# Optimization experiments

Hardware: AMD Instinct MI355X
Metric: run time of the kernel (lower is better)

## Reference

```python
import jax, jax.numpy as jnp
import numpy as np

H, FH, D = 8, 4, 64          # num_heads, focal_heads, att_size
HID = H * D                   # hidden_size = 512
B, S = 8, 512                 # batch, num_nodes
T_HOP, T_EDGE = 32, 16
SCALE = D ** -0.5


def setup_inputs() -> dict:
    key = jax.random.key(0)
    ks = jax.random.split(key, 24)
    f = lambda i, shape: jax.random.normal(ks[i], shape, jnp.float32)
    w = 1.0 / np.sqrt(HID)
    inp = {
        'q': f(0, (B, S, HID)), 'k': f(1, (B, S, HID)), 'v': f(2, (B, S, HID)),
        'query_hop_emb': f(3, (T_HOP, HID)) * 0.02,
        'query_edge_emb': f(4, (T_EDGE, HID)) * 0.02,
        'key_hop_emb': f(5, (T_HOP, HID)) * 0.02,
        'key_edge_emb': f(6, (T_EDGE, HID)) * 0.02,
        'value_hop_emb': f(7, (T_HOP, HID)) * 0.02,
        'value_edge_emb': f(8, (T_EDGE, HID)) * 0.02,
        'distance': jax.random.randint(ks[9], (B, S, S), 0, T_HOP),
        'edge_attr': jax.random.randint(ks[10], (B, S, S), 0, T_EDGE),
        # guarantee at least one unmasked key per query row to keep softmax finite
        'mask': jax.random.bernoulli(ks[11], 0.9, (B, S)).at[:, 0].set(True),
        'focal_mask': jax.random.bernoulli(ks[12], 0.5, (B, S, S)).at[:, :, 0].set(True),
        'Wq': f(13, (HID, H * D)) * w, 'bq': f(14, (H * D,)) * 0.01,
        'Wk': f(15, (HID, H * D)) * w, 'bk': f(16, (H * D,)) * 0.01,
        'Wv': f(17, (HID, H * D)) * w, 'bv': f(18, (H * D,)) * 0.01,
        'Wo': f(19, (H * D, HID)) * w, 'bo': f(20, (HID,)) * 0.01,
    }
    return inp


def _emb_scores(x, emb):
    # x: [B,H,S,D], emb: [T, H*D] -> per-head scores [B,H,S,T]
    e = emb.reshape(-1, H, D).transpose(1, 0, 2)  # [H,T,D]
    return jnp.einsum('bhsd,htd->bhst', x, e)


def _gather_last(scores, idx):
    # scores: [B,H,S,T], idx: [B,S,S] -> [B,H,S,S]
    idx_b = jnp.broadcast_to(idx[:, None], (B, H, S, S))
    return jnp.take_along_axis(scores, idx_b, axis=3)


def _scatter_add_last(attn, idx, T):
    # attn: [B,H,S,S], idx: [B,S,S] -> [B,H,S,T] accumulating attn weights
    idx_b = jnp.broadcast_to(idx[:, None], (B, H, S, S)).reshape(B * H * S, S)
    rows = jnp.arange(B * H * S)[:, None]
    flat = (rows * T + idx_b).reshape(-1)
    out = jnp.zeros((B * H * S * T,), attn.dtype).at[flat].add(attn.reshape(-1))
    return out.reshape(B, H, S, T)


def reference(q, k, v, query_hop_emb, query_edge_emb, key_hop_emb, key_edge_emb,
              value_hop_emb, value_edge_emb, distance, edge_attr, mask, focal_mask,
              Wq, bq, Wk, bk, Wv, bv, Wo, bo):
    qh = (q @ Wq + bq).reshape(B, S, H, D).transpose(0, 2, 1, 3)  # [B,H,S,D]
    kh = (k @ Wk + bk).reshape(B, S, H, D).transpose(0, 2, 1, 3)
    vh = (v @ Wv + bv).reshape(B, S, H, D).transpose(0, 2, 1, 3)

    spatial_bias = (_gather_last(_emb_scores(qh, query_hop_emb), distance)
                    + _gather_last(_emb_scores(kh, key_hop_emb), distance))
    edge_bias = (_gather_last(_emb_scores(qh, query_edge_emb), edge_attr)
                 + _gather_last(_emb_scores(kh, key_edge_emb), edge_attr))

    attn = (jnp.einsum('bhsd,bhtd->bhst', qh, kh) + spatial_bias + edge_bias) * SCALE

    GS = H - FH
    a1 = jnp.where(mask[:, None, None, :], attn[:, :GS], -jnp.inf)
    a2 = jnp.where(focal_mask[:, None], attn[:, GS:], -jnp.inf)
    attn = jax.nn.softmax(jnp.concatenate([a1, a2], axis=1), axis=3)

    vha = _scatter_add_last(attn, distance, T_HOP)   # [B,H,S,T_HOP]
    vea = _scatter_add_last(attn, edge_attr, T_EDGE)  # [B,H,S,T_EDGE]
    vh_emb = value_hop_emb.reshape(T_HOP, H, D).transpose(1, 0, 2)   # [H,T,D]
    ve_emb = value_edge_emb.reshape(T_EDGE, H, D).transpose(1, 0, 2)

    x = (jnp.einsum('bhst,bhtd->bhsd', attn, vh)
         + jnp.einsum('bhst,htd->bhsd', vha, vh_emb)
         + jnp.einsum('bhst,htd->bhsd', vea, ve_emb))
    x = x.transpose(0, 2, 1, 3).reshape(B, S, H * D)
    return x @ Wo + bo
```

## Files before the change

kernel.cpp:

```cpp
#include <hip/hip_runtime.h>

constexpr int nB = 8, nS = 512, nH = 8, nD = 64, nHID = 512;
constexpr int THOP = 32, TEDGE = 16;
constexpr float SCALE = 0.125f;
constexpr float NEGINF = -30000.0f;

typedef __attribute__((ext_vector_type(8))) short bf16x8;
typedef __attribute__((ext_vector_type(4))) float f32x4;

#define MFMA16(A, B, C) __builtin_amdgcn_mfma_f32_16x16x32_bf16(A, B, C, 0, 0, 0)

__device__ __align__(16) unsigned short g_qhi[(size_t)nB * nH * nS * nD];
__device__ __align__(16) unsigned short g_qlo[(size_t)nB * nH * nS * nD];
__device__ __align__(16) unsigned short g_khi[(size_t)nB * nH * nS * nD];
__device__ __align__(16) unsigned short g_klo[(size_t)nB * nH * nS * nD];
__device__ __align__(16) unsigned short g_vhiT[(size_t)nB * nH * nD * nS];
__device__ __align__(16) unsigned short g_vloT[(size_t)nB * nH * nD * nS];
__device__ __align__(16) unsigned short g_embh[96 * 512];
__device__ __align__(16) unsigned short g_embl[96 * 512];
__device__ __align__(16) unsigned short g_inhi[(size_t)3 * 2097152];
__device__ __align__(16) unsigned short g_inlo[(size_t)3 * 2097152];
__device__ __align__(16) unsigned short g_wth[(size_t)4 * 262144];
__device__ __align__(16) unsigned short g_wtl[(size_t)4 * 262144];
__device__ __align__(16) unsigned short g_xhi[(size_t)nB * nS * nHID];
__device__ __align__(16) unsigned short g_xlo[(size_t)nB * nS * nHID];
__device__ int g_flags[32];

__device__ __forceinline__ float ldf(const void* p, int isf32, size_t i) {
  if (isf32) return ((const float*)p)[i];
  unsigned int w = (unsigned int)(((const unsigned short*)p)[i]) << 16;
  return __uint_as_float(w);
}
__device__ __forceinline__ float bf2f(unsigned short h) {
  return __uint_as_float((unsigned)h << 16);
}
__device__ __forceinline__ float4 ldf4(const void* p, int isf32, size_t i) {
  if (isf32) return ((const float4*)p)[i >> 2];
  const ushort4 u = ((const ushort4*)p)[i >> 2];
  float4 r;
  r.x = bf2f(u.x); r.y = bf2f(u.y); r.z = bf2f(u.z); r.w = bf2f(u.w);
  return r;
}
__device__ __forceinline__ unsigned short f2bf(float x) {
  unsigned u = __float_as_uint(x);
  u += 0x7FFFu + ((u >> 16) & 1u);
  return (unsigned short)(u >> 16);
}

__device__ int detect_bool_mode(const unsigned char* p) {
  if (p[0] == 0x80 && p[1] == 0x3F) return 2;
  if (p[0] == 0x00 && p[1] == 0x3C) return 4;
  if (p[0] == 0x00 && p[3] == 0x3F) return 3;
  for (int i = 0; i < 64; i += 4)
    if (p[i + 1] | p[i + 2] | p[i + 3]) return 1;
  return 0;
}
__device__ __forceinline__ bool bool_at(const unsigned char* p, int mode, size_t i) {
  switch (mode) {
    case 0: return ((const int*)p)[i] != 0;
    case 1: return p[i] != 0;
    case 3: return ((const float*)p)[i] != 0.f;
    default: return ((const unsigned short*)p)[i] != 0;
  }
}

__global__ __launch_bounds__(256) void detect_all(
    const void* q, const void* k, const void* v,
    const void* qhe, const void* qee, const void* khe, const void* kee,
    const void* vhe, const void* vee,
    const int* dist, const int* edge,
    const unsigned char* mraw, const unsigned char* fraw,
    const void* Wq, const void* bq, const void* Wk, const void* bk,
    const void* Wv, const void* bv, const void* Wo, const void* bo) {
  __shared__ float sred[256];
  __shared__ int nzs;
  const int tid = threadIdx.x;
  const int blk = blockIdx.x;

  if (blk < 17) {
    const void* arrs[17] = {q, k, v, qhe, qee, khe, kee, vhe, vee,
                            Wq, bq, Wk, bk, Wv, bv, Wo, bo};
    const int full[17] = {2097152, 2097152, 2097152, 8192, 8192, 8192, 8192,
                          8192, 8192, 262144, 512, 262144, 512, 262144, 512,
                          262144, 512};
    const int n = full[blk] < 16384 ? full[blk] : 16384;
    const unsigned short* u = (const unsigned short*)arrs[blk];
    float m = 0.f;
    for (int i = tid; i < n; i += 256) {
      float x = __uint_as_float((unsigned int)u[i] << 16);
      if (x != x) x = 1e20f;
      m = fmaxf(m, fabsf(x));
    }
    sred[tid] = m;
    __syncthreads();
    for (int s = 128; s > 0; s >>= 1) {
      if (tid < s) sred[tid] = fmaxf(sred[tid], sred[tid + s]);
      __syncthreads();
    }
    if (tid == 0) g_flags[4 + blk] = (sred[0] > 1e3f) ? 1 : 0;
  } else if (blk == 17 || blk == 18) {
    const int* p = (blk == 17) ? dist : edge;
    if (tid == 0) nzs = 0;
    __syncthreads();
    int a = 0;
    for (int i = tid; i < 4096; i += 256) a |= p[2 * i + 1];
    if (a) atomicOr(&nzs, 1);
    __syncthreads();
    if (tid == 0) g_flags[blk - 17] = (nzs == 0);
  } else {
    if (tid == 0) {
      g_flags[2] = detect_bool_mode(mraw);
      g_flags[3] = detect_bool_mode(fraw);
    }
  }
}

__global__ __launch_bounds__(256) void emb_prep(
    const void* qhe, const void* khe, const void* qee, const void* kee) {
  const int blk = blockIdx.x;
  const void* srcs[4] = {qhe, khe, qee, kee};
  const int flagIdx[4] = {7, 9, 8, 10};
  const int counts[4] = {32 * 512, 32 * 512, 16 * 512, 16 * 512};
  const int dsts[4] = {0, 32 * 512, 64 * 512, 80 * 512};
  const int f = g_flags[flagIdx[blk]];
  const void* src = srcs[blk];
  const int n = counts[blk], d0 = dsts[blk];
  for (int i = threadIdx.x; i < n; i += 256) {
    const float x = ldf(src, f, i);
    const unsigned short hi = f2bf(x);
    g_embh[d0 + i] = hi;
    g_embl[d0 + i] = f2bf(x - bf2f(hi));
  }
}

__global__ __launch_bounds__(256) void split_prep(
    const void* q, const void* k, const void* v) {
  const int t = blockIdx.y;
  const void* srcs[3] = {q, k, v};
  const int f = g_flags[4 + t];
  const size_t base = (size_t)t * 2097152;
  const size_t i = ((size_t)blockIdx.x * 256 + threadIdx.x) * 4;
  const float4 v4 = ldf4(srcs[t], f, i);
  ushort4 h4, l4;
  h4.x = f2bf(v4.x); l4.x = f2bf(v4.x - bf2f(h4.x));
  h4.y = f2bf(v4.y); l4.y = f2bf(v4.y - bf2f(h4.y));
  h4.z = f2bf(v4.z); l4.z = f2bf(v4.z - bf2f(h4.z));
  h4.w = f2bf(v4.w); l4.w = f2bf(v4.w - bf2f(h4.w));
  *(ushort4*)&g_inhi[base + i] = h4;
  *(ushort4*)&g_inlo[base + i] = l4;
}

__global__ __launch_bounds__(256) void wt_prep(
    const void* Wq, const void* Wk, const void* Wv, const void* Wo) {
  __shared__ float t[64][65];
  const int mat = blockIdx.y;
  const void* srcs[4] = {Wq, Wk, Wv, Wo};
  const int fIdx[4] = {13, 15, 17, 19};
  const int f = g_flags[fIdx[mat]];
  const void* W = srcs[mat];
  const int k0 = (blockIdx.x >> 3) * 64, n0 = (blockIdx.x & 7) * 64;
  const int tid = threadIdx.x;
  const int r = tid >> 4, c4 = (tid & 15) * 4;
#pragma unroll
  for (int i = 0; i < 4; ++i) {
    const float4 v4 = ldf4(W, f, (size_t)(k0 + r + i * 16) * 512 + n0 + c4);
    t[r + i * 16][c4] = v4.x;
    t[r + i * 16][c4 + 1] = v4.y;
    t[r + i * 16][c4 + 2] = v4.z;
    t[r + i * 16][c4 + 3] = v4.w;
  }
  __syncthreads();
  unsigned short* dh = g_wth + (size_t)mat * 262144;
  unsigned short* dl = g_wtl + (size_t)mat * 262144;
#pragma unroll
  for (int i = 0; i < 4; ++i) {
    const int rn = r + i * 16;
    ushort4 h4, l4;
    const float v0 = t[c4][rn], v1 = t[c4 + 1][rn];
    const float v2 = t[c4 + 2][rn], v3 = t[c4 + 3][rn];
    h4.x = f2bf(v0); l4.x = f2bf(v0 - bf2f(h4.x));
    h4.y = f2bf(v1); l4.y = f2bf(v1 - bf2f(h4.y));
    h4.z = f2bf(v2); l4.z = f2bf(v2 - bf2f(h4.z));
    h4.w = f2bf(v3); l4.w = f2bf(v3 - bf2f(h4.w));
    *(ushort4*)&dh[(size_t)(n0 + rn) * 512 + k0 + c4] = h4;
    *(ushort4*)&dl[(size_t)(n0 + rn) * 512 + k0 + c4] = l4;
  }
}

template <int MODE_SEL>
__device__ __forceinline__ void gemm_body(
    const unsigned short* Ahi, const unsigned short* Alo,
    const unsigned short* Wth, const unsigned short* Wtl,
    const void* bias, int bF, float* dst, int mode, int m0, int n0) {
  __shared__ unsigned short As_hi[64][40];
  __shared__ unsigned short As_lo[64][40];
  __shared__ unsigned short Wt_hi[64][40];
  __shared__ unsigned short Wt_lo[64][40];
  const int tid = threadIdx.x;
  const int w = tid >> 6, l = tid & 63, c = l & 15, g = l >> 4;
  const int wr = w >> 1, wc = w & 1;
  const int sr = tid >> 2, sc = (tid & 3) * 8;

  f32x4 acc[2][2] = {{{0.f, 0.f, 0.f, 0.f}, {0.f, 0.f, 0.f, 0.f}},
                     {{0.f, 0.f, 0.f, 0.f}, {0.f, 0.f, 0.f, 0.f}}};

  const size_t ga = (size_t)(m0 + sr) * 512 + sc;
  const size_t gw = (size_t)(n0 + sr) * 512 + sc;
  bf16x8 pa_h = *(const bf16x8*)(Ahi + ga);
  bf16x8 pa_l = *(const bf16x8*)(Alo + ga);
  bf16x8 pw_h = *(const bf16x8*)(Wth + gw);
  bf16x8 pw_l = *(const bf16x8*)(Wtl + gw);

  for (int k0 = 0; k0 < 512; k0 += 32) {
    __syncthreads();
    *(bf16x8*)&As_hi[sr][sc] = pa_h;
    *(bf16x8*)&As_lo[sr][sc] = pa_l;
    *(bf16x8*)&Wt_hi[sr][sc] = pw_h;
    *(bf16x8*)&Wt_lo[sr][sc] = pw_l;
    __syncthreads();
    if (k0 < 480) {
      pa_h = *(const bf16x8*)(Ahi + ga + k0 + 32);
      pa_l = *(const bf16x8*)(Alo + ga + k0 + 32);
      pw_h = *(const bf16x8*)(Wth + gw + k0 + 32);
      pw_l = *(const bf16x8*)(Wtl + gw + k0 + 32);
    }
#pragma unroll
    for (int mi = 0; mi < 2; ++mi) {
      const bf16x8 ah = *(const bf16x8*)&As_hi[wr * 32 + mi * 16 + c][g * 8];
      const bf16x8 al = *(const bf16x8*)&As_lo[wr * 32 + mi * 16 + c][g * 8];
#pragma unroll
      for (int nj = 0; nj < 2; ++nj) {
        const bf16x8 wh = *(const bf16x8*)&Wt_hi[wc * 32 + nj * 16 + c][g * 8];
        const bf16x8 wl = *(const bf16x8*)&Wt_lo[wc * 32 + nj * 16 + c][g * 8];
        acc[mi][nj] = MFMA16(ah, wh, acc[mi][nj]);
        acc[mi][nj] = MFMA16(al, wh, acc[mi][nj]);
        acc[mi][nj] = MFMA16(ah, wl, acc[mi][nj]);
      }
    }
  }
#pragma unroll
  for (int mi = 0; mi < 2; ++mi)
#pragma unroll
    for (int nj = 0; nj < 2; ++nj)
#pragma unroll
      for (int r = 0; r < 4; ++r) {
        const int m = m0 + wr * 32 + mi * 16 + 4 * g + r;
        const int n = n0 + wc * 32 + nj * 16 + c;
        const float v2 = acc[mi][nj][r] + ldf(bias, bF, n);
        if (MODE_SEL == 3) {
          dst[(size_t)m * 512 + n] = v2;
        } else {
          const int b = m >> 9, s = m & 511, h = n >> 6, d = n & 63;
          const unsigned short hi = f2bf(v2);
          const unsigned short lo = f2bf(v2 - bf2f(hi));
          if (mode == 0) {
            const size_t i0 = (((size_t)(b * nH + h) * nS) + s) * nD + d;
            g_qhi[i0] = hi; g_qlo[i0] = lo;
          } else if (mode == 1) {
            const size_t i0 = (((size_t)(b * nH + h) * nS) + s) * nD + d;
            g_khi[i0] = hi; g_klo[i0] = lo;
          } else {
            const size_t i0 = (((size_t)(b * nH + h) * nD) + d) * nS + s;
            g_vhiT[i0] = hi; g_vloT[i0] = lo;
          }
        }
      }
}

__global__ __launch_bounds__(256, 4) void gemm_qkv(
    const unsigned short* __restrict__ inhi, const unsigned short* __restrict__ inlo,
    const unsigned short* __restrict__ wth, const unsigned short* __restrict__ wtl,
    const void* __restrict__ bq, const void* __restrict__ bk,
    const void* __restrict__ bv) {
  const int mat = blockIdx.y >> 6;
  const int m0 = (blockIdx.y & 63) * 64, n0 = blockIdx.x * 64;
  const void* bias = (mat == 0) ? bq : (mat == 1) ? bk : bv;
  const int bF = g_flags[14 + 2 * mat];
  gemm_body<0>(inhi + (size_t)mat * 2097152, inlo + (size_t)mat * 2097152,
               wth + (size_t)mat * 262144, wtl + (size_t)mat * 262144,
               bias, bF, nullptr, mat, m0, n0);
}

__global__ __launch_bounds__(256, 4) void gemm_out(
    const unsigned short* __restrict__ Ahi, const unsigned short* __restrict__ Alo,
    const unsigned short* __restrict__ Wth, const unsigned short* __restrict__ Wtl,
    const void* __restrict__ bias, float* __restrict__ dst) {
  gemm_body<3>(Ahi, Alo, Wth, Wtl, bias, g_flags[20], dst, 3,
               blockIdx.y * 64, blockIdx.x * 64);
}

__global__ __launch_bounds__(256, 4) void attn_kernel(
    const int* __restrict__ dist, const int* __restrict__ edge,
    const unsigned char* __restrict__ mraw, const unsigned char* __restrict__ fraw,
    const void* __restrict__ vhe, const void* __restrict__ vee) {
  __shared__ unsigned short kvbuf[8192];
  __shared__ unsigned short plds[16][520];
  __shared__ float chop_s[16][33];
  __shared__ float cedge_s[16][17];
  __shared__ float vha_s[16][33];
  __shared__ float vea_s[16][17];
  __shared__ float red_s[16][4];
  __shared__ float red2_s[16][4];
  __shared__ float rinv_s[16];

  const int id = blockIdx.x;
  const int bh = (id & 7) * 8 + ((id >> 3) & 7);
  const int qt = id >> 6;
  const int b = bh >> 3, h = bh & 7;
  const int q0 = qt * 16;
  const int tid = threadIdx.x;
  const int w = tid >> 6, l = tid & 63, c = l & 15, g = l >> 4;

  const int d64 = g_flags[0], e64 = g_flags[1];
  const int mmode = g_flags[2], fmode = g_flags[3];
  const int fvhe = g_flags[11], fvee = g_flags[12];

  for (int i = tid; i < 16 * 33; i += 256) (&vha_s[0][0])[i] = 0.f;
  for (int i = tid; i < 16 * 17; i += 256) (&vea_s[0][0])[i] = 0.f;

  auto stageK = [&](int ch) {
#pragma unroll
    for (int it = 0; it < 2; ++it) {
      const int e = (tid << 3) + (it << 11);
      const int r = e >> 6, d0 = e & 63;
      const size_t src = (((size_t)bh * nS) + ch * 64 + r) * nD + d0;
      const int dsti = (r << 6) + (((d0 >> 3) ^ (r & 7)) << 3);
      *(bf16x8*)&kvbuf[dsti] = *(const bf16x8*)(g_khi + src);
      *(bf16x8*)&kvbuf[4096 + dsti] = *(const bf16x8*)(g_klo + src);
    }
  };
  auto stageV = [&](int p) {
#pragma unroll
    for (int it = 0; it < 4; ++it) {
      const int e = (tid << 3) + (it << 11);
      const int d = e >> 7, colc = e & 127;
      const size_t src = (((size_t)bh * nD) + d) * nS + (p << 7) + colc;
      const int dsti = (d << 7) + (((colc >> 3) ^ (d & 15)) << 3);
      *(bf16x8*)&kvbuf[dsti] = *(const bf16x8*)(g_vhiT + src);
    }
  };

  const size_t rowbase = ((size_t)b * nS + q0) * nS;
  for (int j4 = tid; j4 < 2048; j4 += 256) {
    const int j = j4 * 4, r = j >> 9, c1 = j & 511;
    int dv[4], ev[4];
    if (!d64) {
      const int4 t = ((const int4*)(dist + rowbase))[j4];
      dv[0] = t.x & 31; dv[1] = t.y & 31; dv[2] = t.z & 31; dv[3] = t.w & 31;
    } else {
      const int4 t0 = ((const int4*)(dist + 2 * rowbase))[2 * j4];
      const int4 t1 = ((const int4*)(dist + 2 * rowbase))[2 * j4 + 1];
      dv[0] = t0.x & 31; dv[1] = t0.z & 31; dv[2] = t1.x & 31; dv[3] = t1.z & 31;
    }
    if (!e64) {
      const int4 t = ((const int4*)(edge + rowbase))[j4];
      ev[0] = t.x & 15; ev[1] = t.y & 15; ev[2] = t.z & 15; ev[3] = t.w & 15;
    } else {
      const int4 t0 = ((const int4*)(edge + 2 * rowbase))[2 * j4];
      const int4 t1 = ((const int4*)(edge + 2 * rowbase))[2 * j4 + 1];
      ev[0] = t0.x & 15; ev[1] = t0.z & 15; ev[2] = t1.x & 15; ev[3] = t1.z & 15;
    }
    ushort4 pw;
    unsigned short* pp = (unsigned short*)&pw;
#pragma unroll
    for (int t = 0; t < 4; ++t) {
      const bool keep = (h < 4) ? bool_at(mraw, mmode, (size_t)b * nS + c1 + t)
                                : bool_at(fraw, fmode, rowbase + j + t);
      pp[t] = (unsigned short)(dv[t] | (ev[t] << 5) | ((int)keep << 9));
    }
    *(ushort4*)&plds[r][c1] = pw;
  }

  const size_t qbase = (((size_t)bh * nS) + q0 + c) * nD + g * 8;
  const bf16x8 qh0 = *(const bf16x8*)(g_qhi + qbase);
  const bf16x8 qh1 = *(const bf16x8*)(g_qhi + qbase + 32);
  const bf16x8 ql0 = *(const bf16x8*)(g_qlo + qbase);
  const bf16x8 ql1 = *(const bf16x8*)(g_qlo + qbase + 32);

  if (w < 3) {
    const bool isEdge = (w == 2);
    const int tb = (w == 1) ? 16 : 0;
    const size_t qe0 = (isEdge ? (size_t)64 * 512 : 0) + (size_t)(tb + c) * 512 + h * 64;
    const size_t ke0 = (isEdge ? (size_t)80 * 512 : (size_t)32 * 512) + (size_t)(tb + c) * 512 + h * 64;
    f32x4 acc = {0.f, 0.f, 0.f, 0.f};
#pragma unroll
    for (int dh = 0; dh < 2; ++dh) {
      const bf16x8 qhh = dh ? qh1 : qh0;
      const bf16x8 qll = dh ? ql1 : ql0;
      const bf16x8 khq = *(const bf16x8*)(g_khi + qbase + dh * 32);
      const bf16x8 klq = *(const bf16x8*)(g_klo + qbase + dh * 32);
      const bf16x8 eqh = *(const bf16x8*)(g_embh + qe0 + dh * 32 + g * 8);
      const bf16x8 eql = *(const bf16x8*)(g_embl + qe0 + dh * 32 + g * 8);
      const bf16x8 ekh = *(const bf16x8*)(g_embh + ke0 + dh * 32 + g * 8);
      const bf16x8 ekl = *(const bf16x8*)(g_embl + ke0 + dh * 32 + g * 8);
      acc = MFMA16(qhh, eqh, acc);
      acc = MFMA16(qll, eqh, acc);
      acc = MFMA16(qhh, eql, acc);
      acc = MFMA16(khq, ekh, acc);
      acc = MFMA16(klq, ekh, acc);
      acc = MFMA16(khq, ekl, acc);
    }
    if (!isEdge) {
#pragma unroll
      for (int r = 0; r < 4; ++r) chop_s[4 * g + r][tb + c] = acc[r];
    } else {
#pragma unroll
      for (int r = 0; r < 4; ++r) cedge_s[4 * g + r][c] = acc[r];
    }
  }

  stageK(0);
  __syncthreads();

  f32x4 pS[8];
  const int sw8 = c & 7;
  for (int ch = 0; ch < 8; ++ch) {
    const int a0 = (w * 16 + c) << 6;
    f32x4 acc = {0.f, 0.f, 0.f, 0.f};
    {
      const int o0 = a0 + ((g ^ sw8) << 3);
      const int o1 = a0 + (((4 + g) ^ sw8) << 3);
      const bf16x8 kh0 = *(const bf16x8*)&kvbuf[o0];
      const bf16x8 kl0 = *(const bf16x8*)&kvbuf[4096 + o0];
      const bf16x8 kh1 = *(const bf16x8*)&kvbuf[o1];
      const bf16x8 kl1 = *(const bf16x8*)&kvbuf[4096 + o1];
      acc = MFMA16(kh0, qh0, acc);
      acc = MFMA16(kl0, qh0, acc);
      acc = MFMA16(kh0, ql0, acc);
      acc = MFMA16(kh1, qh1, acc);
      acc = MFMA16(kl1, qh1, acc);
      acc = MFMA16(kh1, ql1, acc);
    }
    const int key0 = ch * 64 + w * 16 + 4 * g;
    const ushort4 pv4 = *(const ushort4*)&plds[c][key0];
    const unsigned short pp[4] = {pv4.x, pv4.y, pv4.z, pv4.w};
#pragma unroll
    for (int r = 0; r < 4; ++r) {
      const float s = (acc[r] + chop_s[c][pp[r] & 31] +
                       cedge_s[c][(pp[r] >> 5) & 15]) * SCALE;
      pS[ch][r] = (pp[r] & 512) ? s : NEGINF;
    }
    __syncthreads();
    if (ch < 7) {
      stageK(ch + 1);
      __syncthreads();
    }
  }

  float mx = NEGINF;
#pragma unroll
  for (int kt = 0; kt < 8; ++kt)
#pragma unroll
    for (int r = 0; r < 4; ++r) mx = fmaxf(mx, pS[kt][r]);
  mx = fmaxf(mx, __shfl_xor(mx, 16));
  mx = fmaxf(mx, __shfl_xor(mx, 32));
  if (l < 16) red_s[c][w] = mx;
  stageV(0);
  __syncthreads();
  const float M = fmaxf(fmaxf(red_s[c][0], red_s[c][1]),
                        fmaxf(red_s[c][2], red_s[c][3]));
  float sum = 0.f;
#pragma unroll
  for (int kt = 0; kt < 8; ++kt) {
    const int key0 = kt * 64 + w * 16 + 4 * g;
    const ushort4 pv4 = *(const ushort4*)&plds[c][key0];
    const unsigned short pp[4] = {pv4.x, pv4.y, pv4.z, pv4.w};
#pragma unroll
    for (int r = 0; r < 4; ++r) {
      const float pv = __expf(pS[kt][r] - M);
      pS[kt][r] = pv;
      sum += pv;
      atomicAdd(&vha_s[c][pp[r] & 31], pv);
      atomicAdd(&vea_s[c][(pp[r] >> 5) & 15], pv);
    }
  }
  sum += __shfl_xor(sum, 16);
  sum += __shfl_xor(sum, 32);
  if (l < 16) red2_s[c][w] = sum;
  int pk[8][2];
#pragma unroll
  for (int kt = 0; kt < 8; ++kt) {
    pk[kt][0] = ((int)f2bf(pS[kt][1]) << 16) | (int)f2bf(pS[kt][0]);
    pk[kt][1] = ((int)f2bf(pS[kt][3]) << 16) | (int)f2bf(pS[kt][2]);
  }
  __syncthreads();
  float (*x_s)[17] = reinterpret_cast<float(*)[17]>(&plds[0][0]);
  for (int i = tid; i < 64 * 17; i += 256) (&x_s[0][0])[i] = 0.f;
  if (w == 0 && l < 16) {
    const float tot = red2_s[c][0] + red2_s[c][1] + red2_s[c][2] + red2_s[c][3];
    rinv_s[c] = 1.0f / tot;
  }
  __syncthreads();

  f32x4 oacc[4] = {{0.f, 0.f, 0.f, 0.f}, {0.f, 0.f, 0.f, 0.f},
                   {0.f, 0.f, 0.f, 0.f}, {0.f, 0.f, 0.f, 0.f}};
  const int srcA = ((g & 1) * 2) * 16 + c;
  const int srcB = srcA + 16;
  const bool hi2 = (g >> 1) != 0;
  for (int p = 0; p < 4; ++p) {
    const int t0d0 = __shfl(pk[2 * p][0], srcA);
    const int t1d0 = __shfl(pk[2 * p + 1][0], srcA);
    const int t0d1 = __shfl(pk[2 * p][1], srcA);
    const int t1d1 = __shfl(pk[2 * p + 1][1], srcA);
    const int t0d0b = __shfl(pk[2 * p][0], srcB);
    const int t1d0b = __shfl(pk[2 * p + 1][0], srcB);
    const int t0d1b = __shfl(pk[2 * p][1], srcB);
    const int t1d1b = __shfl(pk[2 * p + 1][1], srcB);
    union { int i[4]; bf16x8 v; } bu;
    bu.i[0] = hi2 ? t1d0 : t0d0;
    bu.i[1] = hi2 ? t1d1 : t0d1;
    bu.i[2] = hi2 ? t1d0b : t0d0b;
    bu.i[3] = hi2 ? t1d1b : t0d1b;
    const int col16 = (w << 1) + (g & 1) + ((g >> 1) << 3);
    const int j0 = (p << 7) + ((g >> 1) << 6) + (w << 4) + ((g & 1) << 3);
#pragma unroll
    for (int t = 0; t < 4; ++t) {
      const int row = t * 16 + c;
      const bf16x8 vh_ = *(const bf16x8*)&kvbuf[(row << 7) + ((col16 ^ c) << 3)];
      const bf16x8 vl_ = *(const bf16x8*)(g_vloT + (((size_t)bh * nD) + row) * nS + j0);
      oacc[t] = MFMA16(vh_, bu.v, oacc[t]);
      oacc[t] = MFMA16(vl_, bu.v, oacc[t]);
    }
    __syncthreads();
    if (p < 3) {
      stageV(p + 1);
      __syncthreads();
    }
  }
#pragma unroll
  for (int t = 0; t < 4; ++t)
#pragma unroll
    for (int r = 0; r < 4; ++r)
      atomicAdd(&x_s[t * 16 + 4 * g + r][c], oacc[t][r]);
  __syncthreads();

  {
    const int d = tid & 63, qq = tid >> 6;
    float val[4];
#pragma unroll
    for (int j = 0; j < 4; ++j) val[j] = x_s[d][qq + 4 * j];
    for (int t = 0; t < THOP; ++t) {
      const float e = ldf(vhe, fvhe, (size_t)t * nHID + h * 64 + d);
#pragma unroll
      for (int j = 0; j < 4; ++j) val[j] += vha_s[qq + 4 * j][t] * e;
    }
    for (int t = 0; t < TEDGE; ++t) {
      const float e = ldf(vee, fvee, (size_t)t * nHID + h * 64 + d);
#pragma unroll
      for (int j = 0; j < 4; ++j) val[j] += vea_s[qq + 4 * j][t] * e;
    }
#pragma unroll
    for (int j = 0; j < 4; ++j) {
      const int q = qq + 4 * j;
      const float xv = val[j] * rinv_s[q];
      const unsigned short hi = f2bf(xv);
      const size_t i0 = ((size_t)b * nS + q0 + q) * nHID + h * 64 + d;
      g_xhi[i0] = hi;
      g_xlo[i0] = f2bf(xv - bf2f(hi));
    }
  }
}

extern "C" void kernel_launch(void* const* d_in, const int* in_sizes, int n_in,
                              void* d_out, int out_size, void* d_ws, size_t ws_size,
                              hipStream_t stream) {
  const void* q   = d_in[0];
  const void* k   = d_in[1];
  const void* v   = d_in[2];
  const void* qhe = d_in[3];
  const void* qee = d_in[4];
  const void* khe = d_in[5];
  const void* kee = d_in[6];
  const void* vhe = d_in[7];
  const void* vee = d_in[8];
  const int* dist = (const int*)d_in[9];
  const int* edge = (const int*)d_in[10];
  const unsigned char* mraw = (const unsigned char*)d_in[11];
  const unsigned char* fraw = (const unsigned char*)d_in[12];
  const void* Wq = d_in[13];
  const void* bq = d_in[14];
  const void* Wk = d_in[15];
  const void* bk = d_in[16];
  const void* Wv = d_in[17];
  const void* bv = d_in[18];
  const void* Wo = d_in[19];
  const void* bo = d_in[20];

  detect_all<<<20, 256, 0, stream>>>(q, k, v, qhe, qee, khe, kee, vhe, vee,
                                     dist, edge, mraw, fraw,
                                     Wq, bq, Wk, bk, Wv, bv, Wo, bo);
  emb_prep<<<4, 256, 0, stream>>>(qhe, khe, qee, kee);
  split_prep<<<dim3(2048, 3), 256, 0, stream>>>(q, k, v);
  wt_prep<<<dim3(64, 4), 256, 0, stream>>>(Wq, Wk, Wv, Wo);

  unsigned short* inhi; hipGetSymbolAddress((void**)&inhi, HIP_SYMBOL(g_inhi));
  unsigned short* inlo; hipGetSymbolAddress((void**)&inlo, HIP_SYMBOL(g_inlo));
  unsigned short* wth;  hipGetSymbolAddress((void**)&wth,  HIP_SYMBOL(g_wth));
  unsigned short* wtl;  hipGetSymbolAddress((void**)&wtl,  HIP_SYMBOL(g_wtl));
  unsigned short* xhi;  hipGetSymbolAddress((void**)&xhi,  HIP_SYMBOL(g_xhi));
  unsigned short* xlo;  hipGetSymbolAddress((void**)&xlo,  HIP_SYMBOL(g_xlo));

  gemm_qkv<<<dim3(8, 192), 256, 0, stream>>>(inhi, inlo, wth, wtl, bq, bk, bv);
  attn_kernel<<<2048, 256, 0, stream>>>(dist, edge, mraw, fraw, vhe, vee);
  gemm_out<<<dim3(8, 64), 256, 0, stream>>>(xhi, xlo,
                                            wth + 3 * 262144, wtl + 3 * 262144,
                                            bo, (float*)d_out);
}
```

Measured before the change: 609.9 us.

## Prefetch next K/V chunk into registers before compute in attention loop

Splits the K and V staging into separate global-load and LDS-write steps. The next chunk's global loads are issued into registers at the start of each iteration so their latency overlaps the MFMA work, and the registers are written to shared memory after the barrier. Launch bounds drop from 4 to 3 blocks per SM to make room for the extra prefetch registers, which may reduce occupancy.

```diff
diff --git a/kernel.cpp b/kernel.cpp
--- a/kernel.cpp
+++ b/kernel.cpp
@@ -289,7 +289,7 @@
                blockIdx.y * 64, blockIdx.x * 64);
 }
 
-__global__ __launch_bounds__(256, 4) void attn_kernel(
+__global__ __launch_bounds__(256, 3) void attn_kernel(
     const int* __restrict__ dist, const int* __restrict__ edge,
     const unsigned char* __restrict__ mraw, const unsigned char* __restrict__ fraw,
     const void* __restrict__ vhe, const void* __restrict__ vee) {
@@ -318,27 +318,43 @@
   for (int i = tid; i < 16 * 33; i += 256) (&vha_s[0][0])[i] = 0.f;
   for (int i = tid; i < 16 * 17; i += 256) (&vea_s[0][0])[i] = 0.f;
 
-  auto stageK = [&](int ch) {
-#pragma unroll
-    for (int it = 0; it < 2; ++it) {
-      const int e = (tid << 3) + (it << 11);
-      const int r = e >> 6, d0 = e & 63;
-      const size_t src = (((size_t)bh * nS) + ch * 64 + r) * nD + d0;
-      const int dsti = (r << 6) + (((d0 >> 3) ^ (r & 7)) << 3);
-      *(bf16x8*)&kvbuf[dsti] = *(const bf16x8*)(g_khi + src);
-      *(bf16x8*)&kvbuf[4096 + dsti] = *(const bf16x8*)(g_klo + src);
-    }
+  const int e0 = tid << 3;
+  const int kr0 = e0 >> 6, kd0 = e0 & 63;
+  const int vd0 = e0 >> 7, vcol = e0 & 127;
+  bf16x8 rkh0, rkh1, rkl0, rkl1;
+  bf16x8 rv0, rv1, rv2, rv3;
+
+  auto loadK = [&](int ch) {
+    const size_t base = ((size_t)bh * nS + ch * 64) * nD + kd0;
+    rkh0 = *(const bf16x8*)(g_khi + base + (size_t)kr0 * nD);
+    rkl0 = *(const bf16x8*)(g_klo + base + (size_t)kr0 * nD);
+    rkh1 = *(const bf16x8*)(g_khi + base + (size_t)(kr0 + 32) * nD);
+    rkl1 = *(const bf16x8*)(g_klo + base + (size_t)(kr0 + 32) * nD);
   };
-  auto stageV = [&](int p) {
-#pragma unroll
-    for (int it = 0; it < 4; ++it) {
-      const int e = (tid << 3) + (it << 11);
-      const int d = e >> 7, colc = e & 127;
-      const size_t src = (((size_t)bh * nD) + d) * nS + (p << 7) + colc;
-      const int dsti = (d << 7) + (((colc >> 3) ^ (d & 15)) << 3);
-      *(bf16x8*)&kvbuf[dsti] = *(const bf16x8*)(g_vhiT + src);
-    }
+  auto writeK = [&]() {
+    const int dst0 = (kr0 << 6) + (((kd0 >> 3) ^ (kr0 & 7)) << 3);
+    const int dst1 = ((kr0 + 32) << 6) + (((kd0 >> 3) ^ ((kr0 + 32) & 7)) << 3);
+    *(bf16x8*)&kvbuf[dst0] = rkh0;
+    *(bf16x8*)&kvbuf[4096 + dst0] = rkl0;
+    *(bf16x8*)&kvbuf[dst1] = rkh1;
+    *(bf16x8*)&kvbuf[4096 + dst1] = rkl1;
   };
+  auto loadV = [&](int p) {
+    const size_t base = (size_t)bh * nD * nS + (p << 7) + vcol;
+    rv0 = *(const bf16x8*)(g_vhiT + base + (size_t)vd0 * nS);
+    rv1 = *(const bf16x8*)(g_vhiT + base + (size_t)(vd0 + 16) * nS);
+    rv2 = *(const bf16x8*)(g_vhiT + base + (size_t)(vd0 + 32) * nS);
+    rv3 = *(const bf16x8*)(g_vhiT + base + (size_t)(vd0 + 48) * nS);
+  };
+  auto writeV = [&]() {
+    const int swz = ((vcol >> 3) ^ (vd0 & 15)) << 3;
+    *(bf16x8*)&kvbuf[(vd0 << 7) + swz] = rv0;
+    *(bf16x8*)&kvbuf[((vd0 + 16) << 7) + swz] = rv1;
+    *(bf16x8*)&kvbuf[((vd0 + 32) << 7) + swz] = rv2;
+    *(bf16x8*)&kvbuf[((vd0 + 48) << 7) + swz] = rv3;
+  };
+
+  loadK(0);
 
   const size_t rowbase = ((size_t)b * nS + q0) * nS;
   for (int j4 = tid; j4 < 2048; j4 += 256) {
@@ -409,12 +425,13 @@
     }
   }
 
-  stageK(0);
+  writeK();
   __syncthreads();
 
   f32x4 pS[8];
   const int sw8 = c & 7;
   for (int ch = 0; ch < 8; ++ch) {
+    if (ch < 7) loadK(ch + 1);
     const int a0 = (w * 16 + c) << 6;
     f32x4 acc = {0.f, 0.f, 0.f, 0.f};
     {
@@ -442,10 +459,12 @@
     }
     __syncthreads();
     if (ch < 7) {
-      stageK(ch + 1);
+      writeK();
       __syncthreads();
     }
   }
+
+  loadV(0);
 
   float mx = NEGINF;
 #pragma unroll
@@ -455,7 +474,6 @@
   mx = fmaxf(mx, __shfl_xor(mx, 16));
   mx = fmaxf(mx, __shfl_xor(mx, 32));
   if (l < 16) red_s[c][w] = mx;
-  stageV(0);
   __syncthreads();
   const float M = fmaxf(fmaxf(red_s[c][0], red_s[c][1]),
                         fmaxf(red_s[c][2], red_s[c][3]));
@@ -483,6 +501,7 @@
     pk[kt][0] = ((int)f2bf(pS[kt][1]) << 16) | (int)f2bf(pS[kt][0]);
     pk[kt][1] = ((int)f2bf(pS[kt][3]) << 16) | (int)f2bf(pS[kt][2]);
   }
+  writeV();
   __syncthreads();
   float (*x_s)[17] = reinterpret_cast<float(*)[17]>(&plds[0][0]);
   for (int i = tid; i < 64 * 17; i += 256) (&x_s[0][0])[i] = 0.f;
@@ -498,6 +517,7 @@
   const int srcB = srcA + 16;
   const bool hi2 = (g >> 1) != 0;
   for (int p = 0; p < 4; ++p) {
+    if (p < 3) loadV(p + 1);
     const int t0d0 = __shfl(pk[2 * p][0], srcA);
     const int t1d0 = __shfl(pk[2 * p + 1][0], srcA);
     const int t0d1 = __shfl(pk[2 * p][1], srcA);
@@ -523,7 +543,7 @@
     }
     __syncthreads();
     if (p < 3) {
-      stageV(p + 1);
+      writeV();
       __syncthreads();
     }
   }
```

Result: faster. 558.4 us (-8.4%).
